# Optimization experiments

Measured on AMD Instinct MI355X. Metric: run time of the kernel, lower is better.

The kernel has to match this reference:

```python
import jax, jax.numpy as jnp
import numpy as np

# Episode config: 4 episodes, 5-way 5-shot, 15 queries/class, 84x84 RGB
B, NTR, NTE, K = 4, 25, 75, 5
H = W = 84
CH = (64, 64, 128, 512)   # 4-block conv backbone channels
NUM_CLASSES = 64
SCALE_CLS = 1.0
EPS = 1e-12


def _l2norm(x, axis):
    # matches torch F.normalize(p=2, eps=1e-12)
    n = jnp.sqrt(jnp.sum(x * x, axis=axis, keepdims=True))
    return x / jnp.maximum(n, EPS)


def _conv_block(x, w, b):
    y = jax.lax.conv_general_dilated(x, w, (1, 1), 'SAME',
                                     dimension_numbers=('NCHW', 'OIHW', 'NCHW'))
    y = jax.nn.relu(y + b[None, :, None, None])
    return jax.lax.reduce_window(y, -jnp.inf, jax.lax.max,
                                 (1, 1, 2, 2), (1, 1, 2, 2), 'VALID')


def _backbone(x, ws, bs):
    for w, b in zip(ws, bs):
        x = _conv_block(x, w, b)
    return x  # (N, 512, 5, 5)


def setup_inputs() -> dict:
    key = jax.random.key(0)
    ks = jax.random.split(key, 16)
    xtrain = jax.random.normal(ks[0], (B, NTR, 3, H, W), jnp.float32)
    xtest = jax.random.normal(ks[1], (B, NTE, 3, H, W), jnp.float32)
    # one-hot support labels: 5 examples per class
    labels_tr = jnp.tile(jnp.arange(K), NTR // K)  # (NTR,)
    ytrain = jnp.tile(jax.nn.one_hot(labels_tr, K, dtype=jnp.float32)[None], (B, 1, 1))
    ytest = jax.random.randint(ks[2], (B, NTE), 0, K)
    # backbone conv params (He init)
    params = {}
    cin = 3
    for i, cout in enumerate(CH):
        scale = np.sqrt(2.0 / (cin * 9)).astype(np.float32)
        params[f'w{i+1}'] = jax.random.normal(ks[3 + i], (cout, cin, 3, 3), jnp.float32) * scale
        params[f'b{i+1}'] = jnp.zeros((cout,), jnp.float32)
        cin = cout
    params['wc'] = jax.random.normal(ks[10], (NUM_CLASSES, CH[-1]), jnp.float32) * np.sqrt(1.0 / CH[-1]).astype(np.float32)
    params['bc'] = jnp.zeros((NUM_CLASSES,), jnp.float32)
    return {'xtrain': xtrain, 'xtest': xtest, 'ytrain': ytrain, 'ytest': ytest, **params}


def reference(xtrain, xtest, ytrain, ytest,
              w1, b1, w2, b2, w3, b3, w4, b4, wc, bc):
    b, n_tr = xtrain.shape[0], xtrain.shape[1]
    n_te = xtest.shape[1]
    k = ytrain.shape[2]
    x = jnp.concatenate([xtrain.reshape(-1, 3, H, W),
                         xtest.reshape(-1, 3, H, W)], axis=0)
    f = _backbone(x, (w1, w2, w3, w4), (b1, b2, b3, b4))  # (N, c, h, w)
    c, h, w = f.shape[1], f.shape[2], f.shape[3]

    # class-averaged support prototypes (full feature maps)
    ftr = f[:b * n_tr].reshape(b, n_tr, c * h * w)
    yT = jnp.swapaxes(ytrain, 1, 2)                       # (b, k, n_tr)
    ftr = jnp.einsum('bkn,bnd->bkd', yT, ftr) / jnp.sum(yT, axis=2, keepdims=True)
    ftr = ftr.reshape(b, k, c, h, w)

    fte = f[b * n_tr:].reshape(b, n_te, c, h, w)

    # global classifier head on GAP'd, l2-normalized query features
    f_test = _l2norm(jnp.mean(fte, axis=(3, 4)).reshape(b * n_te, c), axis=1)
    predict_test = f_test @ wc.T + bc                     # (b*n_te, 64)

    # pairwise cosine scoring: original materializes (b,n2,n1,c,h,w) repeats;
    # mathematically identical einsum over the channel dim.
    ftr_avg = _l2norm(jnp.mean(ftr, axis=(3, 4)), axis=2)  # (b, k, c)
    fte_n = _l2norm(fte, axis=2)                           # (b, n_te, c, h, w)
    cls_scores = SCALE_CLS * jnp.einsum('bjchw,bic->bjihw', fte_n, ftr_avg)
    cls_scores = cls_scores.reshape(b * n_te, k, h, w)
    return predict_test, cls_scores
```

## Files before the change

### kernel.cpp

```cpp
#include <hip/hip_runtime.h>
#include <hip/hip_bf16.h>

#define DEV __device__ __forceinline__

typedef __attribute__((ext_vector_type(8))) short bf16x8;
typedef __attribute__((ext_vector_type(4))) short bf16x4;
typedef __attribute__((ext_vector_type(4))) float f32x4;

DEV unsigned short f2bf(float v) {
    union { __hip_bfloat16 b; unsigned short u; } c;
    c.b = __float2bfloat16(v);
    return c.u;
}

#define OFF_X1P   0
#define OFF_X2P   99123200
#define OFF_X3P   126208000
#define OFF_W1T   140953600
#define OFF_W2T   140964096
#define OFF_W3T   141056256
#define OFF_W4T   141240576
#define OFF_F4    0
#define OFF_G     20480000
#define OFF_PROTO 21299200

template<int HP, int WP, int C>
DEV void ring_zero(short* __restrict__ Xp, int img)
{
    constexpr int RING = 2 * WP + 2 * (HP - 2);
    constexpr int U = C / 8;
    short* base = Xp + (size_t)img * (HP * WP * C);
    uint4 z; z.x = z.y = z.z = z.w = 0;
    for (int i = threadIdx.x; i < RING * U; i += 256) {
        int r = i / U, u = i % U;
        int y, x;
        if (r < WP)            { y = 0;      x = r; }
        else if (r < 2 * WP)   { y = HP - 1; x = r - WP; }
        else { int s = r - 2 * WP; y = 1 + (s >> 1); x = (s & 1) ? (WP - 1) : 0; }
        *(uint4*)(base + ((size_t)(y * WP + x)) * C + u * 8) = z;
    }
}

__global__ __launch_bounds__(256)
void border_zero_all_kernel(short* __restrict__ X1p, short* __restrict__ X2p,
                            short* __restrict__ X3p)
{
    int b = blockIdx.x;
    if (b < 400)      ring_zero<44, 44, 64>(X1p, b);
    else if (b < 800) ring_zero<23, 23, 64>(X2p, b - 400);
    else              ring_zero<12, 12, 128>(X3p, b - 800);
}

template<int COUT, int CIN>
DEV void wt_tap_elem(const float* __restrict__ w, short* __restrict__ dst, int t)
{
    int cout = t / (CIN * 9), k = t % (CIN * 9);
    int tap = k / CIN, cin = k % CIN;
    float v = w[((size_t)cout * CIN + cin) * 9 + tap];
    dst[((size_t)(k >> 5) * COUT + cout) * 40 + (k & 31)] = (short)f2bf(v);
}

__global__ __launch_bounds__(256)
void wt_all_kernel(const float* __restrict__ w1, const float* __restrict__ w2,
                   const float* __restrict__ w3, const float* __restrict__ w4,
                   short* __restrict__ W1t, short* __restrict__ W2t,
                   short* __restrict__ W3t, short* __restrict__ W4t)
{
    int t = blockIdx.x * 256 + threadIdx.x;
    if (t < 5120) {
        int cout = t / 80, kk = t % 80;
        int tap = kk >> 2, cin = kk & 3;
        float v = (tap < 9 && cin < 3) ? w1[(cout * 3 + cin) * 9 + tap] : 0.f;
        W1t[cout * 80 + kk] = (short)f2bf(v);
        return;
    }
    t -= 5120;
    if (t < 36864) { wt_tap_elem<64, 64>(w2, W2t, t); return; }
    t -= 36864;
    if (t < 73728) { wt_tap_elem<128, 64>(w3, W3t, t); return; }
    t -= 73728;
    if (t < 589824) wt_tap_elem<512, 128>(w4, W4t, t);
}

__global__ __launch_bounds__(256, 2)
void conv1_mfma_kernel(const float* __restrict__ xtrain, const float* __restrict__ xtest,
                       const short* __restrict__ W1t, const float* __restrict__ bias,
                       short* __restrict__ X1p)
{
    constexpr int RSTR = 352;
    __shared__ short sr[8 * RSTR];
    __shared__ float sb[64];

    const int tid = threadIdx.x;
    const int img = blockIdx.x / 14, blkrow = blockIdx.x % 14;
    const int yp0 = blkrow * 3;
    const float* src = (img < 100) ? xtrain + (size_t)img * (3 * 84 * 84)
                                   : xtest  + (size_t)(img - 100) * (3 * 84 * 84);
    const int wv = tid >> 6, lane = tid & 63, quad = lane >> 4, ln = lane & 15;

    for (int i = tid; i < 8 * 86; i += 256) {
        int r = i / 86, c = i % 86;
        int gy = 2 * yp0 - 1 + r, gx = c - 1;
        bf16x4 v = (bf16x4)0;
        if (gy >= 0 && gy < 84 && gx >= 0 && gx < 84) {
            int o = gy * 84 + gx;
            v[0] = (short)f2bf(src[o]);
            v[1] = (short)f2bf(src[7056 + o]);
            v[2] = (short)f2bf(src[14112 + o]);
        }
        *(bf16x4*)(&sr[r * RSTR + c * 4]) = v;
    }
    if (tid < 64) sb[tid] = bias[tid];

    const int t0 = 2 * quad, t1 = 2 * quad + 1;
    const int off0 = (t0 / 3) * RSTR + (t0 % 3) * 4;
    const int off1 = (t1 / 3) * RSTR + (t1 % 3) * 4;
    const int off2 = 2 * RSTR + 2 * 4;

    bf16x8 af0[4], af1[4];
    #pragma unroll
    for (int mi = 0; mi < 4; ++mi) {
        af0[mi] = *(const bf16x8*)(W1t + (mi * 16 + ln) * 80 + quad * 8);
        af1[mi] = *(const bf16x8*)(W1t + (mi * 16 + ln) * 80 + 32 + quad * 8);
    }

    f32x4 acc[4][8];
    #pragma unroll
    for (int mi = 0; mi < 4; ++mi)
        #pragma unroll
        for (int ni = 0; ni < 8; ++ni) acc[mi][ni] = (f32x4)0.f;

    __syncthreads();

    #pragma unroll
    for (int ni = 0; ni < 8; ++ni) {
        int q = wv * 128 + ni * 16 + ln;
        int qc = (q < 504) ? q : 503;
        int ypl = qc / 168, rem = qc % 168;
        int x = rem >> 1, dy = rem & 1;
        int base = (2 * ypl + dy) * RSTR + x * 4;

        bf16x4 lo0 = *(const bf16x4*)(&sr[base + off0]);
        bf16x4 hi0 = *(const bf16x4*)(&sr[base + off1]);
        bf16x8 b0;
        #pragma unroll
        for (int j = 0; j < 4; ++j) { b0[j] = lo0[j]; b0[4 + j] = hi0[j]; }
        bf16x4 lo1 = *(const bf16x4*)(&sr[base + off2]);
        bf16x8 b1;
        #pragma unroll
        for (int j = 0; j < 4; ++j) { b1[j] = lo1[j]; b1[4 + j] = lo1[j]; }

        #pragma unroll
        for (int mi = 0; mi < 4; ++mi) {
            acc[mi][ni] = __builtin_amdgcn_mfma_f32_16x16x32_bf16(b0, af0[mi], acc[mi][ni], 0, 0, 0);
            acc[mi][ni] = __builtin_amdgcn_mfma_f32_16x16x32_bf16(b1, af1[mi], acc[mi][ni], 0, 0, 0);
        }
    }

    #pragma unroll
    for (int ni = 0; ni < 8; ++ni) {
        int g = wv * 32 + ni * 4 + quad;
        bool ok = (g < 126);
        int ypl = g / 42, xg = g % 42;
        #pragma unroll
        for (int mi = 0; mi < 4; ++mi) {
            f32x4 a = acc[mi][ni];
            float m = fmaxf(fmaxf(a[0], a[1]), fmaxf(a[2], a[3]));
            if (ok) {
                int cout = mi * 16 + ln;
                unsigned short h = f2bf(fmaxf(m + sb[cout], 0.f));
                int py = yp0 + ypl;
                size_t o = (((size_t)img * 44 + py + 1) * 44 + xg + 1) * 64 + cout;
                X1p[o] = (short)h;
            }
        }
    }
}

template<int CIN, int COUT, int NWM, int NWN, int MT, int NT, int YPB,
         int WOUT, int HPIN, int WPIN, int HPO, int WPO, int RBI>
__global__ __launch_bounds__(256, 2)
void conv_mfma_kernel(const short* __restrict__ Xp, const short* __restrict__ Wt,
                      const float* __restrict__ bias, short* __restrict__ Yp)
{
    constexpr int ROWS = 2 * YPB + 2, CSTR = CIN + 8;
    constexpr int KC = CIN * 9 / 32, CPT = CIN / 32;
    constexpr int WPAIR = (2 * WOUT + 3) / 4 * 4;
    constexpr int NSLOT = YPB * WPAIR, POOLW = WOUT / 2;
    constexpr int GPR = WPAIR / 4;
    static_assert(KC % 6 == 0, "KC must divide 6");
    __shared__ short sx[ROWS * WPIN * CSTR];
    __shared__ float sb[COUT];

    const int tid = threadIdx.x;
    const int img = blockIdx.x / RBI, blkrow = blockIdx.x % RBI;
    const int yp0 = blkrow * YPB;
    const int wv = tid >> 6, lane = tid & 63, quad = lane >> 4, ln = lane & 15;
    const int msup = (NWM == 1) ? 0 : (wv >> 1);
    const int nsup = (NWM == 1) ? wv : (wv & 1);

    const short* xsrc = Xp + ((size_t)img * HPIN + 2 * yp0) * (WPIN * CIN);
    for (int i = tid; i < ROWS * WPIN * (CIN / 8); i += 256) {
        int g = i % (CIN / 8), pc = i / (CIN / 8);
        uint4 v = *(const uint4*)(xsrc + (size_t)pc * CIN + g * 8);
        *(uint4*)(&sx[pc * CSTR + g * 8]) = v;
    }
    for (int i = tid; i < COUT; i += 256) sb[i] = bias[i];

    int pbase[NT];
    #pragma unroll
    for (int ni = 0; ni < NT; ++ni) {
        int q = nsup * (NT * 16) + ni * 16 + ln;
        int qc = (q < NSLOT) ? q : (NSLOT - 1);
        int ypl = qc / WPAIR, rem = qc % WPAIR;
        int x = rem >> 1; if (x > WOUT - 1) x = WOUT - 1;
        int dy = rem & 1;
        pbase[ni] = (((2 * ypl + dy) * WPIN + x) * CSTR + quad * 8) * 2;
    }

    f32x4 acc[MT][NT];
    #pragma unroll
    for (int mi = 0; mi < MT; ++mi)
        #pragma unroll
        for (int ni = 0; ni < NT; ++ni) acc[mi][ni] = (f32x4)0.f;

    auto loadAF = [&](bf16x8* dst, int kc) {
        #pragma unroll
        for (int mi = 0; mi < MT; ++mi)
            dst[mi] = *(const bf16x8*)(Wt + ((size_t)kc * COUT + msup * 64 + mi * 16 + ln) * 40 + quad * 8);
    };
    auto loadBF = [&](bf16x8* dst, int kc) {
        const int tap = kc / CPT, cb = (kc % CPT) * 32;
        const int ky = tap / 3, kx = tap % 3;
        const int koff = ((ky * WPIN + kx) * CSTR + cb) * 2;
        #pragma unroll
        for (int ni = 0; ni < NT; ++ni)
            dst[ni] = *(const bf16x8*)((const char*)sx + pbase[ni] + koff);
    };

    __syncthreads();

    bf16x8 af[3][MT], bf[2][NT];
    loadAF(af[0], 0); loadAF(af[1], 1); loadBF(bf[0], 0);
    for (int kc = 0; kc < KC; kc += 6) {
        #pragma unroll
        for (int j = 0; j < 6; ++j) {
            int ka = kc + j + 2; if (ka > KC - 1) ka = KC - 1;
            int kb = kc + j + 1; if (kb > KC - 1) kb = KC - 1;
            loadAF(af[(j + 2) % 3], ka);
            loadBF(bf[(j + 1) & 1], kb);
            #pragma unroll
            for (int mi = 0; mi < MT; ++mi)
                #pragma unroll
                for (int ni = 0; ni < NT; ++ni)
                    acc[mi][ni] = __builtin_amdgcn_mfma_f32_16x16x32_bf16(
                        bf[j & 1][ni], af[j % 3][mi], acc[mi][ni], 0, 0, 0);
        }
    }

    #pragma unroll
    for (int ni = 0; ni < NT; ++ni) {
        int g = nsup * (NT * 4) + ni * 4 + quad;
        int ypl = g / GPR, xg = g % GPR;
        bool ok = (g < NSLOT / 4) && (xg < POOLW);
        #pragma unroll
        for (int mi = 0; mi < MT; ++mi) {
            f32x4 a = acc[mi][ni];
            float m = fmaxf(fmaxf(a[0], a[1]), fmaxf(a[2], a[3]));
            if (ok) {
                int cout = msup * 64 + mi * 16 + ln;
                unsigned short h = f2bf(fmaxf(m + sb[cout], 0.f));
                int py = yp0 + ypl;
                Yp[(((size_t)img * HPO + py + 1) * WPO + xg + 1) * COUT + cout] = (short)h;
            }
        }
    }
}

__global__ __launch_bounds__(256, 2)
void conv4_mfma_kernel(const short* __restrict__ X3p, const short* __restrict__ W4t,
                       const float* __restrict__ bias, float* __restrict__ f4)
{
    constexpr int CSTR = 136;
    __shared__ short sx[144 * CSTR];
    __shared__ float sb[128];

    const int tid = threadIdx.x;
    const int img = blockIdx.x >> 2, mb = blockIdx.x & 3;
    const int wv = tid >> 6, lane = tid & 63, quad = lane >> 4, ln = lane & 15;
    const int msup = wv >> 1, nsup = wv & 1;

    const short* xsrc = X3p + (size_t)img * (144 * 128);
    for (int i = tid; i < 144 * 16; i += 256) {
        int pc = i >> 4, g = i & 15;
        uint4 v = *(const uint4*)(xsrc + pc * 128 + g * 8);
        *(uint4*)(&sx[pc * CSTR + g * 8]) = v;
    }
    for (int i = tid; i < 128; i += 256) sb[i] = bias[mb * 128 + i];

    int pbase[4];
    #pragma unroll
    for (int ni = 0; ni < 4; ++ni) {
        int q = nsup * 64 + ni * 16 + ln;
        int pc = (q < 100) ? q : 99;
        int yp = pc / 20, rem = pc % 20;
        int y = 2 * yp + (rem & 1), x = rem >> 1;
        pbase[ni] = ((y * 12 + x) * CSTR + quad * 8) * 2;
    }

    f32x4 acc[4][4];
    #pragma unroll
    for (int mi = 0; mi < 4; ++mi)
        #pragma unroll
        for (int ni = 0; ni < 4; ++ni) acc[mi][ni] = (f32x4)0.f;

    auto loadAF = [&](bf16x8* dst, int kc) {
        #pragma unroll
        for (int mi = 0; mi < 4; ++mi)
            dst[mi] = *(const bf16x8*)(W4t + ((size_t)kc * 512 + mb * 128 + msup * 64 + mi * 16 + ln) * 40 + quad * 8);
    };
    auto loadBF = [&](bf16x8* dst, int kc) {
        const int tap = kc >> 2, cb = (kc & 3) * 32;
        const int ky = tap / 3, kx = tap % 3;
        const int koff = ((ky * 12 + kx) * CSTR + cb) * 2;
        #pragma unroll
        for (int ni = 0; ni < 4; ++ni)
            dst[ni] = *(const bf16x8*)((const char*)sx + pbase[ni] + koff);
    };

    __syncthreads();

    bf16x8 af[3][4], bf[2][4];
    loadAF(af[0], 0); loadAF(af[1], 1); loadBF(bf[0], 0);
    for (int kc = 0; kc < 36; kc += 6) {
        #pragma unroll
        for (int j = 0; j < 6; ++j) {
            int ka = kc + j + 2; if (ka > 35) ka = 35;
            int kb = kc + j + 1; if (kb > 35) kb = 35;
            loadAF(af[(j + 2) % 3], ka);
            loadBF(bf[(j + 1) & 1], kb);
            #pragma unroll
            for (int mi = 0; mi < 4; ++mi)
                #pragma unroll
                for (int ni = 0; ni < 4; ++ni)
                    acc[mi][ni] = __builtin_amdgcn_mfma_f32_16x16x32_bf16(
                        bf[j & 1][ni], af[j % 3][mi], acc[mi][ni], 0, 0, 0);
        }
    }

    #pragma unroll
    for (int ni = 0; ni < 4; ++ni) {
        int g = nsup * 16 + ni * 4 + quad;
        bool ok = (g < 25);
        #pragma unroll
        for (int mi = 0; mi < 4; ++mi) {
            f32x4 a = acc[mi][ni];
            float m = fmaxf(fmaxf(a[0], a[1]), fmaxf(a[2], a[3]));
            if (ok) {
                int cl = msup * 64 + mi * 16 + ln;
                f4[((size_t)img * 25 + g) * 512 + mb * 128 + cl] = fmaxf(m + sb[cl], 0.f);
            }
        }
    }
}

__global__ __launch_bounds__(256)
void gap_kernel(const float* __restrict__ f4, float* __restrict__ g)
{
    const int img = blockIdx.x;
    for (int c = threadIdx.x; c < 512; c += 256) {
        float s = 0.f;
        #pragma unroll
        for (int p = 0; p < 25; ++p)
            s += f4[((size_t)img * 25 + p) * 512 + c];
        g[(size_t)img * 512 + c] = s * (1.f / 25.f);
    }
}

__global__ __launch_bounds__(256)
void proto_kernel(const float* __restrict__ g, const float* __restrict__ ytrain,
                  float* __restrict__ proto)
{
    const int b = blockIdx.x / 5, k = blockIdx.x % 5;
    __shared__ float sp[512];
    __shared__ float red[256];

    float yv[25];
    float cnt = 0.f;
    for (int n = 0; n < 25; ++n) {
        yv[n] = ytrain[(size_t)(b * 25 + n) * 5 + k];
        cnt += yv[n];
    }
    const float icnt = 1.f / cnt;

    for (int c = threadIdx.x; c < 512; c += 256) {
        float s = 0.f;
        for (int n = 0; n < 25; ++n)
            s += yv[n] * g[((size_t)(b * 25 + n)) * 512 + c];
        sp[c] = s * icnt;
    }
    __syncthreads();

    float ss = 0.f;
    for (int c = threadIdx.x; c < 512; c += 256) ss += sp[c] * sp[c];
    red[threadIdx.x] = ss;
    __syncthreads();
    for (int s = 128; s > 0; s >>= 1) {
        if (threadIdx.x < s) red[threadIdx.x] += red[threadIdx.x + s];
        __syncthreads();
    }
    const float inv = 1.f / fmaxf(sqrtf(red[0]), 1e-12f);
    for (int c = threadIdx.x; c < 512; c += 256)
        proto[((size_t)(b * 5 + k)) * 512 + c] = sp[c] * inv;
}

__global__ __launch_bounds__(64)
void predict_kernel(const float* __restrict__ g, const float* __restrict__ wc,
                    const float* __restrict__ bc, float* __restrict__ out)
{
    const int q = blockIdx.x;
    __shared__ float fq[512];
    const float* gq = g + (size_t)(100 + q) * 512;
    float ss = 0.f;
    for (int c = threadIdx.x; c < 512; c += 64) {
        const float v = gq[c];
        fq[c] = v;
        ss += v * v;
    }
    #pragma unroll
    for (int o = 32; o > 0; o >>= 1) ss += __shfl_down(ss, o);
    const float inv = 1.f / fmaxf(sqrtf(__shfl(ss, 0)), 1e-12f);
    __syncthreads();

    const int m = threadIdx.x;
    float s = bc[m];
    for (int c = 0; c < 512; ++c)
        s = fmaf(fq[c] * inv, wc[m * 512 + c], s);
    out[q * 64 + m] = s;
}

__global__ __launch_bounds__(256)
void cls_kernel(const float* __restrict__ f4, const float* __restrict__ proto,
                float* __restrict__ outc)
{
    __shared__ float sf[25 * 516];
    __shared__ float spr[5 * 516];
    const int q = blockIdx.x, b = q / 75;
    const float* f = f4 + (size_t)(100 + q) * (25 * 512);
    for (int i = threadIdx.x; i < 3200; i += 256) {
        int row = i >> 7, col = i & 127;
        *(float4*)(&sf[row * 516 + col * 4]) = *(const float4*)(f + row * 512 + col * 4);
    }
    const float* pb = proto + (size_t)b * 5 * 512;
    for (int i = threadIdx.x; i < 640; i += 256) {
        int row = i >> 7, col = i & 127;
        *(float4*)(&spr[row * 516 + col * 4]) = *(const float4*)(pb + row * 512 + col * 4);
    }
    __syncthreads();

    for (int it = threadIdx.x; it < 125; it += 256) {
        int i = it / 25, p = it % 25;
        const float* fp = &sf[p * 516];
        const float* pr = &spr[i * 516];
        float ss = 0.f, dot = 0.f;
        for (int c = 0; c < 512; c += 4) {
            float4 v = *(const float4*)(fp + c);
            float4 w = *(const float4*)(pr + c);
            ss  += v.x * v.x + v.y * v.y + v.z * v.z + v.w * v.w;
            dot += v.x * w.x + v.y * w.y + v.z * w.z + v.w * w.w;
        }
        outc[(size_t)q * 125 + it] = dot / fmaxf(sqrtf(ss), 1e-12f);
    }
}

extern "C" void kernel_launch(void* const* d_in, const int* in_sizes, int n_in,
                              void* d_out, int out_size, void* d_ws, size_t ws_size,
                              hipStream_t stream)
{
    (void)in_sizes; (void)n_in; (void)out_size; (void)ws_size;
    const float* xtrain = (const float*)d_in[0];
    const float* xtest  = (const float*)d_in[1];
    const float* ytrain = (const float*)d_in[2];
    const float* w1 = (const float*)d_in[4];
    const float* b1 = (const float*)d_in[5];
    const float* w2 = (const float*)d_in[6];
    const float* b2 = (const float*)d_in[7];
    const float* w3 = (const float*)d_in[8];
    const float* b3 = (const float*)d_in[9];
    const float* w4 = (const float*)d_in[10];
    const float* b4 = (const float*)d_in[11];
    const float* wc = (const float*)d_in[12];
    const float* bc = (const float*)d_in[13];

    char* ws = (char*)d_ws;
    short* X1p = (short*)(ws + OFF_X1P);
    short* X2p = (short*)(ws + OFF_X2P);
    short* X3p = (short*)(ws + OFF_X3P);
    short* W1t = (short*)(ws + OFF_W1T);
    short* W2t = (short*)(ws + OFF_W2T);
    short* W3t = (short*)(ws + OFF_W3T);
    short* W4t = (short*)(ws + OFF_W4T);
    float* f4    = (float*)(ws + OFF_F4);
    float* g     = (float*)(ws + OFF_G);
    float* proto = (float*)(ws + OFF_PROTO);
    float* out = (float*)d_out;

    border_zero_all_kernel<<<1200, 256, 0, stream>>>(X1p, X2p, X3p);
    wt_all_kernel<<<2756, 256, 0, stream>>>(w1, w2, w3, w4, W1t, W2t, W3t, W4t);

    conv1_mfma_kernel<<<400 * 14, 256, 0, stream>>>(xtrain, xtest, W1t, b1, X1p);
    conv_mfma_kernel< 64,  64,  1,  4, 4, 4,  3,  42,  44,  44, 23, 23,  7>
        <<<400 * 7, 256, 0, stream>>>(X1p, W2t, b2, X2p);
    conv_mfma_kernel< 64, 128,  2,  2, 4, 7,  5,  21,  23,  23, 12, 12,  2>
        <<<400 * 2, 256, 0, stream>>>(X2p, W3t, b3, X3p);
    conv4_mfma_kernel<<<400 * 4, 256, 0, stream>>>(X3p, W4t, b4, f4);

    gap_kernel<<<400, 256, 0, stream>>>(f4, g);
    proto_kernel<<<20, 256, 0, stream>>>(g, ytrain, proto);
    predict_kernel<<<300, 64, 0, stream>>>(g, wc, bc, out);
    cls_kernel<<<300, 256, 0, stream>>>(f4, proto, out + 19200);
}
```

Baseline: 341.5 us.

## Simplify conv MFMA double-buffering and speed up predict and cls heads

Swaps the 3/2-deep rotating fragment prefetch in the conv MFMA kernels for a plain A/B ping-pong double buffer over pairs of K chunks, and drops the KC%6 requirement. Transposes the classifier weights once in the weight-prep kernel so predict_kernel can read them coalesced, spread over 256 threads with a split-K reduction. Makes cls_kernel compute each query position's norm once instead of five times. The main conv kernels dominate the runtime, and the new prefetch depth may overlap loads with math less than the old scheme did.

Result: faster. 315.9 us (-7.5%).

```diff
diff --git a/kernel.cpp b/kernel.cpp
--- a/kernel.cpp
+++ b/kernel.cpp
@@ -20,6 +20,7 @@
 #define OFF_W2T   140964096
 #define OFF_W3T   141056256
 #define OFF_W4T   141240576
+#define OFF_WCT   142715136
 #define OFF_F4    0
 #define OFF_G     20480000
 #define OFF_PROTO 21299200
@@ -63,8 +64,10 @@
 __global__ __launch_bounds__(256)
 void wt_all_kernel(const float* __restrict__ w1, const float* __restrict__ w2,
                    const float* __restrict__ w3, const float* __restrict__ w4,
+                   const float* __restrict__ wc,
                    short* __restrict__ W1t, short* __restrict__ W2t,
-                   short* __restrict__ W3t, short* __restrict__ W4t)
+                   short* __restrict__ W3t, short* __restrict__ W4t,
+                   float* __restrict__ wcT)
 {
     int t = blockIdx.x * 256 + threadIdx.x;
     if (t < 5120) {
@@ -79,7 +82,12 @@
     t -= 36864;
     if (t < 73728) { wt_tap_elem<128, 64>(w3, W3t, t); return; }
     t -= 73728;
-    if (t < 589824) wt_tap_elem<512, 128>(w4, W4t, t);
+    if (t < 589824) { wt_tap_elem<512, 128>(w4, W4t, t); return; }
+    t -= 589824;
+    if (t < 32768) {
+        int c = t >> 6, m = t & 63;
+        wcT[t] = wc[m * 512 + c];
+    }
 }
 
 __global__ __launch_bounds__(256, 2)
@@ -188,7 +196,6 @@
     constexpr int WPAIR = (2 * WOUT + 3) / 4 * 4;
     constexpr int NSLOT = YPB * WPAIR, POOLW = WOUT / 2;
     constexpr int GPR = WPAIR / 4;
-    static_assert(KC % 6 == 0, "KC must divide 6");
     __shared__ short sx[ROWS * WPIN * CSTR];
     __shared__ float sb[COUT];
 
@@ -240,22 +247,21 @@
 
     __syncthreads();
 
-    bf16x8 af[3][MT], bf[2][NT];
-    loadAF(af[0], 0); loadAF(af[1], 1); loadBF(bf[0], 0);
-    for (int kc = 0; kc < KC; kc += 6) {
-        #pragma unroll
-        for (int j = 0; j < 6; ++j) {
-            int ka = kc + j + 2; if (ka > KC - 1) ka = KC - 1;
-            int kb = kc + j + 1; if (kb > KC - 1) kb = KC - 1;
-            loadAF(af[(j + 2) % 3], ka);
-            loadBF(bf[(j + 1) & 1], kb);
+    bf16x8 afA[MT], afB[MT], bfA[NT], bfB[NT];
+    loadAF(afA, 0); loadBF(bfA, 0);
+    for (int kc = 0; kc < KC; kc += 2) {
+        loadAF(afB, kc + 1); loadBF(bfB, kc + 1);
+        #pragma unroll
+        for (int mi = 0; mi < MT; ++mi)
             #pragma unroll
-            for (int mi = 0; mi < MT; ++mi)
-                #pragma unroll
-                for (int ni = 0; ni < NT; ++ni)
-                    acc[mi][ni] = __builtin_amdgcn_mfma_f32_16x16x32_bf16(
-                        bf[j & 1][ni], af[j % 3][mi], acc[mi][ni], 0, 0, 0);
-        }
+            for (int ni = 0; ni < NT; ++ni)
+                acc[mi][ni] = __builtin_amdgcn_mfma_f32_16x16x32_bf16(bfA[ni], afA[mi], acc[mi][ni], 0, 0, 0);
+        if (kc + 2 < KC) { loadAF(afA, kc + 2); loadBF(bfA, kc + 2); }
+        #pragma unroll
+        for (int mi = 0; mi < MT; ++mi)
+            #pragma unroll
+            for (int ni = 0; ni < NT; ++ni)
+                acc[mi][ni] = __builtin_amdgcn_mfma_f32_16x16x32_bf16(bfB[ni], afB[mi], acc[mi][ni], 0, 0, 0);
     }
 
     #pragma unroll
@@ -330,22 +336,21 @@
 
     __syncthreads();
 
-    bf16x8 af[3][4], bf[2][4];
-    loadAF(af[0], 0); loadAF(af[1], 1); loadBF(bf[0], 0);
-    for (int kc = 0; kc < 36; kc += 6) {
-        #pragma unroll
-        for (int j = 0; j < 6; ++j) {
-            int ka = kc + j + 2; if (ka > 35) ka = 35;
-            int kb = kc + j + 1; if (kb > 35) kb = 35;
-            loadAF(af[(j + 2) % 3], ka);
-            loadBF(bf[(j + 1) & 1], kb);
+    bf16x8 afA[4], afB[4], bfA[4], bfB[4];
+    loadAF(afA, 0); loadBF(bfA, 0);
+    for (int kc = 0; kc < 36; kc += 2) {
+        loadAF(afB, kc + 1); loadBF(bfB, kc + 1);
+        #pragma unroll
+        for (int mi = 0; mi < 4; ++mi)
             #pragma unroll
-            for (int mi = 0; mi < 4; ++mi)
-                #pragma unroll
-                for (int ni = 0; ni < 4; ++ni)
-                    acc[mi][ni] = __builtin_amdgcn_mfma_f32_16x16x32_bf16(
-                        bf[j & 1][ni], af[j % 3][mi], acc[mi][ni], 0, 0, 0);
-        }
+            for (int ni = 0; ni < 4; ++ni)
+                acc[mi][ni] = __builtin_amdgcn_mfma_f32_16x16x32_bf16(bfA[ni], afA[mi], acc[mi][ni], 0, 0, 0);
+        if (kc + 2 < 36) { loadAF(afA, kc + 2); loadBF(bfA, kc + 2); }
+        #pragma unroll
+        for (int mi = 0; mi < 4; ++mi)
+            #pragma unroll
+            for (int ni = 0; ni < 4; ++ni)
+                acc[mi][ni] = __builtin_amdgcn_mfma_f32_16x16x32_bf16(bfB[ni], afB[mi], acc[mi][ni], 0, 0, 0);
     }
 
     #pragma unroll
@@ -414,29 +419,39 @@
         proto[((size_t)(b * 5 + k)) * 512 + c] = sp[c] * inv;
 }
 
-__global__ __launch_bounds__(64)
-void predict_kernel(const float* __restrict__ g, const float* __restrict__ wc,
+__global__ __launch_bounds__(256)
+void predict_kernel(const float* __restrict__ g, const float* __restrict__ wcT,
                     const float* __restrict__ bc, float* __restrict__ out)
 {
     const int q = blockIdx.x;
     __shared__ float fq[512];
+    __shared__ float red[256];
+    __shared__ float part[4][64];
+
     const float* gq = g + (size_t)(100 + q) * 512;
     float ss = 0.f;
-    for (int c = threadIdx.x; c < 512; c += 64) {
+    for (int c = threadIdx.x; c < 512; c += 256) {
         const float v = gq[c];
         fq[c] = v;
         ss += v * v;
     }
-    #pragma unroll
-    for (int o = 32; o > 0; o >>= 1) ss += __shfl_down(ss, o);
-    const float inv = 1.f / fmaxf(sqrtf(__shfl(ss, 0)), 1e-12f);
-    __syncthreads();
-
-    const int m = threadIdx.x;
-    float s = bc[m];
-    for (int c = 0; c < 512; ++c)
-        s = fmaf(fq[c] * inv, wc[m * 512 + c], s);
-    out[q * 64 + m] = s;
+    red[threadIdx.x] = ss;
+    __syncthreads();
+    for (int s = 128; s > 0; s >>= 1) {
+        if (threadIdx.x < s) red[threadIdx.x] += red[threadIdx.x + s];
+        __syncthreads();
+    }
+    const float inv = 1.f / fmaxf(sqrtf(red[0]), 1e-12f);
+
+    const int cp = threadIdx.x >> 6, m = threadIdx.x & 63;
+    float s = 0.f;
+    const int c0 = cp * 128;
+    for (int c = c0; c < c0 + 128; ++c)
+        s = fmaf(fq[c], wcT[c * 64 + m], s);
+    part[cp][m] = s;
+    __syncthreads();
+    if (threadIdx.x < 64)
+        out[q * 64 + m] = (part[0][m] + part[1][m] + part[2][m] + part[3][m]) * inv + bc[m];
 }
 
 __global__ __launch_bounds__(256)
@@ -445,6 +460,7 @@
 {
     __shared__ float sf[25 * 516];
     __shared__ float spr[5 * 516];
+    __shared__ float pinv[25];
     const int q = blockIdx.x, b = q / 75;
     const float* f = f4 + (size_t)(100 + q) * (25 * 512);
     for (int i = threadIdx.x; i < 3200; i += 256) {
@@ -458,18 +474,28 @@
     }
     __syncthreads();
 
+    if (threadIdx.x < 25) {
+        const float* fp = &sf[threadIdx.x * 516];
+        float ss = 0.f;
+        for (int c = 0; c < 512; c += 4) {
+            float4 v = *(const float4*)(fp + c);
+            ss += v.x * v.x + v.y * v.y + v.z * v.z + v.w * v.w;
+        }
+        pinv[threadIdx.x] = 1.f / fmaxf(sqrtf(ss), 1e-12f);
+    }
+    __syncthreads();
+
     for (int it = threadIdx.x; it < 125; it += 256) {
         int i = it / 25, p = it % 25;
         const float* fp = &sf[p * 516];
         const float* pr = &spr[i * 516];
-        float ss = 0.f, dot = 0.f;
+        float dot = 0.f;
         for (int c = 0; c < 512; c += 4) {
             float4 v = *(const float4*)(fp + c);
             float4 w = *(const float4*)(pr + c);
-            ss  += v.x * v.x + v.y * v.y + v.z * v.z + v.w * v.w;
             dot += v.x * w.x + v.y * w.y + v.z * w.z + v.w * w.w;
         }
-        outc[(size_t)q * 125 + it] = dot / fmaxf(sqrtf(ss), 1e-12f);
+        outc[(size_t)q * 125 + it] = dot * pinv[p];
     }
 }
 
@@ -500,13 +526,15 @@
     short* W2t = (short*)(ws + OFF_W2T);
     short* W3t = (short*)(ws + OFF_W3T);
     short* W4t = (short*)(ws + OFF_W4T);
+    float* wcT = (float*)(ws + OFF_WCT);
     float* f4    = (float*)(ws + OFF_F4);
     float* g     = (float*)(ws + OFF_G);
     float* proto = (float*)(ws + OFF_PROTO);
     float* out = (float*)d_out;
 
     border_zero_all_kernel<<<1200, 256, 0, stream>>>(X1p, X2p, X3p);
-    wt_all_kernel<<<2756, 256, 0, stream>>>(w1, w2, w3, w4, W1t, W2t, W3t, W4t);
+    wt_all_kernel<<<2884, 256, 0, stream>>>(w1, w2, w3, w4, wc,
+                                            W1t, W2t, W3t, W4t, wcT);
 
     conv1_mfma_kernel<<<400 * 14, 256, 0, stream>>>(xtrain, xtest, W1t, b1, X1p);
     conv_mfma_kernel< 64,  64,  1,  4, 4, 4,  3,  42,  44,  44, 23, 23,  7>
@@ -517,6 +545,6 @@
 
     gap_kernel<<<400, 256, 0, stream>>>(f4, g);
     proto_kernel<<<20, 256, 0, stream>>>(g, ytrain, proto);
-    predict_kernel<<<300, 64, 0, stream>>>(g, wc, bc, out);
+    predict_kernel<<<300, 256, 0, stream>>>(g, wcT, bc, out);
     cls_kernel<<<300, 256, 0, stream>>>(f4, proto, out + 19200);
 }
```
